# Kernel tuning notes

Measured on AMD Instinct MI355X. Metric: run time of the kernel, lower is better.

Reference implementation:

```python
import jax, jax.numpy as jnp
import numpy as np
import math

NUM_IN_C = 128      # rep_2d num_c (c_z)
ATT_C = 64          # attention_num_c
NUM_HEADS = 4
B, T, I, J = 1, 4, 256, 256


def setup_inputs() -> dict:
    key = jax.random.key(0)
    ks = jax.random.split(key, 7)
    s = 1.0 / math.sqrt(NUM_IN_C)
    return {
        "z2d": jax.random.normal(ks[0], (B, I, J, NUM_IN_C), dtype=jnp.float32),
        "t2d": jax.random.normal(ks[1], (B, T, I, J, NUM_IN_C), dtype=jnp.float32),
        # nn.Linear weights are [out_features, in_features]; apply as x @ W.T
        "Wq": jax.random.normal(ks[2], (ATT_C * NUM_HEADS, NUM_IN_C), dtype=jnp.float32) * s,
        "Wk": jax.random.normal(ks[3], (ATT_C * NUM_HEADS, NUM_IN_C), dtype=jnp.float32) * s,
        "Wv": jax.random.normal(ks[4], (ATT_C * NUM_HEADS, NUM_IN_C), dtype=jnp.float32) * s,
        "Wo": jax.random.normal(ks[5], (NUM_IN_C, ATT_C * NUM_HEADS), dtype=jnp.float32) * s,
        "bo": jax.random.normal(ks[6], (NUM_IN_C,), dtype=jnp.float32) * 0.02,
    }


def reference(z2d, t2d, Wq, Wk, Wv, Wo, bo):
    # Projections; reshape last dim to (attention_num_c, num_heads) per torch .view
    q = (z2d @ Wq.T).reshape(*z2d.shape[:-1], ATT_C, NUM_HEADS)        # b i j c h
    k = (t2d @ Wk.T).reshape(*t2d.shape[:-1], ATT_C, NUM_HEADS)        # b t i j c h
    v = (t2d @ Wv.T).reshape(*t2d.shape[:-1], ATT_C, NUM_HEADS)        # b t i j c h
    # NOTE: original scales by sqrt(num_in_c), not sqrt(attention_num_c)
    scores = jnp.einsum('bijch,btijch->btijh', q, k) / math.sqrt(NUM_IN_C)
    w = jax.nn.softmax(scores, axis=1)                                  # softmax over template axis t
    out = jnp.einsum('btijh,btijch->bijch', w, v)                       # b i j c h
    out = out.reshape(*out.shape[:-2], ATT_C * NUM_HEADS)               # flatten (c,h)
    return out @ Wo.T + bo
```

## Files before the change

### kernel.cpp

```cpp
#include <hip/hip_runtime.h>


#define PIX 65536
#define MT 32

typedef __attribute__((ext_vector_type(8))) short s8v;
typedef __attribute__((ext_vector_type(4))) float f4v;
typedef __attribute__((ext_vector_type(4))) unsigned short us4v;
typedef __attribute__((ext_vector_type(4))) float fl4;

__device__ __forceinline__ unsigned short f2bf(float x) {
    unsigned int u = __float_as_uint(x);
    u = (u + 0x7FFFu + ((u >> 16) & 1u)) >> 16;
    return (unsigned short)u;
}
__device__ __forceinline__ float bf2fs(short v) {
    return __uint_as_float(((unsigned int)(unsigned short)v) << 16);
}

__global__ __launch_bounds__(256) void build_weights(
        const float* __restrict__ Wq, const float* __restrict__ Wk,
        const float* __restrict__ Wv, const float* __restrict__ Wo,
        unsigned short* __restrict__ mcat, unsigned short* __restrict__ pcat) {
    int b = blockIdx.x;
    if (b < 256) {
        int idx = b * 256 + threadIdx.x;
        int n = idx >> 7, k1 = idx & 127;
        int h = n >> 7, k2 = n & 127;
        float s = 0.f;
        #pragma unroll 8
        for (int c = 0; c < 64; c++) {
            int r = c * 4 + h;
            s += Wq[r * 128 + k1] * Wk[r * 128 + k2];
        }
        mcat[idx] = f2bf(s * 0.088388347648318447f);
    } else {
        int idx = (b - 256) * 256 + threadIdx.x;
        int m = idx >> 9, kk = idx & 511;
        int h = kk >> 7, k = kk & 127;
        float s = 0.f;
        #pragma unroll 8
        for (int c = 0; c < 64; c++) {
            int r = c * 4 + h;
            s += Wo[m * 256 + r] * Wv[r * 128 + k];
        }
        pcat[idx] = f2bf(s);
    }
}

#define AT_OFS 0
#define U_OFS  17408
#define BUF_USH (17408 + 16768)

__global__ __launch_bounds__(256, 2) void fused_attn(
    const float* __restrict__ z2d, const float* __restrict__ t2d,
    const unsigned short* __restrict__ mcat, const unsigned short* __restrict__ pcat,
    const float* __restrict__ bo, float* __restrict__ out) {

    __shared__ unsigned short buf[BUF_USH];
    __shared__ float Sc[4][32][4];

    const int tid = threadIdx.x;
    const int pbase = blockIdx.x * MT;
    const int wv = tid >> 6, lane = tid & 63, quad = lane >> 4, l15 = lane & 15;
    const int mt = wv & 1;
    const int nsel = wv >> 1;

    s8v za[4];
    {
        const float* zp = z2d + (size_t)(pbase + mt * 16 + l15) * 128 + quad * 8;
        #pragma unroll
        for (int ks = 0; ks < 4; ks++) {
            const fl4 d0 = *(const fl4*)(zp + ks * 32);
            const fl4 d1 = *(const fl4*)(zp + ks * 32 + 4);
            s8v a;
            a[0] = (short)f2bf(d0[0]); a[1] = (short)f2bf(d0[1]);
            a[2] = (short)f2bf(d0[2]); a[3] = (short)f2bf(d0[3]);
            a[4] = (short)f2bf(d1[0]); a[5] = (short)f2bf(d1[1]);
            a[6] = (short)f2bf(d1[2]); a[7] = (short)f2bf(d1[3]);
            za[ks] = a;
        }
    }

    for (int v = tid; v < 4096; v += 256) {
        int t = v >> 10, rem = v & 1023, p = rem >> 5, k4 = (rem & 31) << 2;
        const fl4 d = *(const fl4*)(t2d + ((size_t)t * PIX + pbase + p) * 128 + k4);
        us4v w;
        w[0] = f2bf(d[0]); w[1] = f2bf(d[1]); w[2] = f2bf(d[2]); w[3] = f2bf(d[3]);
        *(us4v*)&buf[AT_OFS + (t * 32 + p) * 136 + k4] = w;
    }
    __syncthreads();

    for (int nblk = 0; nblk < 8; nblk++) {
        s8v b0[4], b1[4];
        #pragma unroll
        for (int ks = 0; ks < 4; ks++) {
            b0[ks] = *(const s8v*)(mcat + (size_t)(nblk * 64 + nsel * 32 + l15) * 128
                                        + ks * 32 + quad * 8);
            b1[ks] = *(const s8v*)(mcat + (size_t)(nblk * 64 + nsel * 32 + 16 + l15) * 128
                                        + ks * 32 + quad * 8);
        }
        f4v acc0 = {0.f, 0.f, 0.f, 0.f}, acc1 = {0.f, 0.f, 0.f, 0.f};
        #pragma unroll
        for (int ks = 0; ks < 4; ks++) {
            acc0 = __builtin_amdgcn_mfma_f32_16x16x32_bf16(za[ks], b0[ks], acc0, 0, 0, 0);
            acc1 = __builtin_amdgcn_mfma_f32_16x16x32_bf16(za[ks], b1[ks], acc1, 0, 0, 0);
        }
        const int prow = mt * 16 + quad * 4;
        const int cb = nblk * 64 + nsel * 32 + l15;
        #pragma unroll
        for (int r = 0; r < 4; r++) {
            buf[U_OFS + (prow + r) * 524 + cb]      = f2bf(acc0[r]);
            buf[U_OFS + (prow + r) * 524 + cb + 16] = f2bf(acc1[r]);
        }
    }
    __syncthreads();

    {
        const int t = wv;
        #pragma unroll
        for (int pt = 0; pt < 2; pt++) {
            s8v bt[4];
            #pragma unroll
            for (int ks = 0; ks < 4; ks++)
                bt[ks] = *(const s8v*)&buf[AT_OFS + (t * 32 + pt * 16 + l15) * 136
                                            + ks * 32 + quad * 8];
            #pragma unroll
            for (int h = 0; h < 4; h++) {
                f4v c = {0.f, 0.f, 0.f, 0.f};
                #pragma unroll
                for (int ks = 0; ks < 4; ks++) {
                    const s8v a = *(const s8v*)&buf[U_OFS + (pt * 16 + l15) * 524
                                                     + h * 128 + ks * 32 + quad * 8];
                    c = __builtin_amdgcn_mfma_f32_16x16x32_bf16(a, bt[ks], c, 0, 0, 0);
                }
                const int rsel = l15 & 3;
                float dv = rsel == 0 ? c[0] : rsel == 1 ? c[1] : rsel == 2 ? c[2] : c[3];
                if ((l15 >> 2) == quad) Sc[t][pt * 16 + l15][h] = dv;
            }
        }
    }
    __syncthreads();

    if (tid < 128) {
        const int p = tid >> 2, h = tid & 3;
        float x0 = Sc[0][p][h], x1 = Sc[1][p][h], x2 = Sc[2][p][h], x3 = Sc[3][p][h];
        float mx = fmaxf(fmaxf(x0, x1), fmaxf(x2, x3));
        float e0 = __expf(x0 - mx), e1 = __expf(x1 - mx);
        float e2 = __expf(x2 - mx), e3 = __expf(x3 - mx);
        float inv = 1.f / (e0 + e1 + e2 + e3);
        Sc[0][p][h] = e0 * inv; Sc[1][p][h] = e1 * inv;
        Sc[2][p][h] = e2 * inv; Sc[3][p][h] = e3 * inv;
    }
    __syncthreads();

    {
        const int p = tid >> 3, seg = tid & 7;
        float w[4][4];
        #pragma unroll
        for (int t = 0; t < 4; t++) {
            const fl4 ww = *(const fl4*)&Sc[t][p][0];
            w[t][0] = ww[0]; w[t][1] = ww[1]; w[t][2] = ww[2]; w[t][3] = ww[3];
        }
        #pragma unroll
        for (int half = 0; half < 2; half++) {
            const int k = seg * 16 + half * 8;
            s8v a[4];
            #pragma unroll
            for (int t = 0; t < 4; t++)
                a[t] = *(const s8v*)&buf[AT_OFS + (t * 32 + p) * 136 + k];
            s8v o[4];
            #pragma unroll
            for (int j = 0; j < 8; j++) {
                const float a0 = bf2fs(a[0][j]), a1 = bf2fs(a[1][j]);
                const float a2 = bf2fs(a[2][j]), a3 = bf2fs(a[3][j]);
                #pragma unroll
                for (int h = 0; h < 4; h++) {
                    o[h][j] = (short)f2bf(w[0][h] * a0 + w[1][h] * a1
                                        + w[2][h] * a2 + w[3][h] * a3);
                }
            }
            #pragma unroll
            for (int h = 0; h < 4; h++)
                *(s8v*)&buf[AT_OFS + (h * 32 + p) * 136 + k] = o[h];
        }
    }
    __syncthreads();

    f4v accd[4];
    #pragma unroll
    for (int i = 0; i < 4; i++) accd[i] = (f4v){0.f, 0.f, 0.f, 0.f};
    #pragma unroll
    for (int h = 0; h < 4; h++) {
        s8v af[4];
        #pragma unroll
        for (int ks = 0; ks < 4; ks++)
            af[ks] = *(const s8v*)&buf[AT_OFS + (h * 32 + mt * 16 + l15) * 136
                                        + ks * 32 + quad * 8];
        #pragma unroll
        for (int nt = 0; nt < 4; nt++) {
            #pragma unroll
            for (int ks = 0; ks < 4; ks++) {
                const s8v b = *(const s8v*)(pcat + (size_t)(nsel * 64 + nt * 16 + l15) * 512
                                                 + h * 128 + ks * 32 + quad * 8);
                accd[nt] = __builtin_amdgcn_mfma_f32_16x16x32_bf16(af[ks], b, accd[nt], 0, 0, 0);
            }
        }
    }

    const int prow2 = mt * 16 + quad * 4;
    #pragma unroll
    for (int nt = 0; nt < 4; nt++) {
        const int m = nsel * 64 + nt * 16 + l15;
        const float bb = bo[m];
        #pragma unroll
        for (int r = 0; r < 4; r++) {
            out[(size_t)(pbase + prow2 + r) * 128 + m] = accd[nt][r] + bb;
        }
    }
}

extern "C" void kernel_launch(void* const* d_in, const int* in_sizes, int n_in,
                              void* d_out, int out_size, void* d_ws, size_t ws_size,
                              hipStream_t stream) {
    const float* z2d = (const float*)d_in[0];
    const float* t2d = (const float*)d_in[1];
    const float* Wq  = (const float*)d_in[2];
    const float* Wk  = (const float*)d_in[3];
    const float* Wv  = (const float*)d_in[4];
    const float* Wo  = (const float*)d_in[5];
    const float* bo  = (const float*)d_in[6];

    unsigned short* mcat = (unsigned short*)d_ws;
    unsigned short* pcat = mcat + 512 * 128;

    build_weights<<<512, 256, 0, stream>>>(Wq, Wk, Wv, Wo, mcat, pcat);
    fused_attn<<<PIX / MT, 256, 0, stream>>>(z2d, t2d, mcat, pcat, bo, (float*)d_out);
}
```

Measured before the change: 343.5 us.

## Halve pixel tile per block and raise occupancy to four blocks per CU

Shrinks the per-block pixel tile from 32 to 16, halving shared memory use, and raises the launch-bounds target from 2 to 4 blocks per CU. The warp-to-work mapping is reorganised so each wave covers all 16 pixels with its own column slice in the projection and output GEMMs. The t2d load loop is fully unrolled. The aim is more resident waves to hide global-load latency, at the cost of reloading weight fragments (mcat/pcat) twice as often per pixel and giving each wave less MFMA work.

```diff
diff --git a/kernel.cpp b/kernel.cpp
--- a/kernel.cpp
+++ b/kernel.cpp
@@ -2,7 +2,7 @@
 
 
 #define PIX 65536
-#define MT 32
+#define MT 16
 
 typedef __attribute__((ext_vector_type(8))) short s8v;
 typedef __attribute__((ext_vector_type(4))) float f4v;
@@ -49,26 +49,24 @@
 }
 
 #define AT_OFS 0
-#define U_OFS  17408
-#define BUF_USH (17408 + 16768)
-
-__global__ __launch_bounds__(256, 2) void fused_attn(
+#define U_OFS  8704
+#define BUF_USH (8704 + 8384)
+
+__global__ __launch_bounds__(256, 4) void fused_attn(
     const float* __restrict__ z2d, const float* __restrict__ t2d,
     const unsigned short* __restrict__ mcat, const unsigned short* __restrict__ pcat,
     const float* __restrict__ bo, float* __restrict__ out) {
 
     __shared__ unsigned short buf[BUF_USH];
-    __shared__ float Sc[4][32][4];
+    __shared__ float Sc[4][16][4];
 
     const int tid = threadIdx.x;
     const int pbase = blockIdx.x * MT;
     const int wv = tid >> 6, lane = tid & 63, quad = lane >> 4, l15 = lane & 15;
-    const int mt = wv & 1;
-    const int nsel = wv >> 1;
 
     s8v za[4];
     {
-        const float* zp = z2d + (size_t)(pbase + mt * 16 + l15) * 128 + quad * 8;
+        const float* zp = z2d + (size_t)(pbase + l15) * 128 + quad * 8;
         #pragma unroll
         for (int ks = 0; ks < 4; ks++) {
             const fl4 d0 = *(const fl4*)(zp + ks * 32);
@@ -82,67 +80,57 @@
         }
     }
 
-    for (int v = tid; v < 4096; v += 256) {
-        int t = v >> 10, rem = v & 1023, p = rem >> 5, k4 = (rem & 31) << 2;
+    #pragma unroll
+    for (int i = 0; i < 8; i++) {
+        int v = i * 256 + tid;
+        int t = v >> 9, rem = v & 511, p = rem >> 5, k4 = (rem & 31) << 2;
         const fl4 d = *(const fl4*)(t2d + ((size_t)t * PIX + pbase + p) * 128 + k4);
         us4v w;
         w[0] = f2bf(d[0]); w[1] = f2bf(d[1]); w[2] = f2bf(d[2]); w[3] = f2bf(d[3]);
-        *(us4v*)&buf[AT_OFS + (t * 32 + p) * 136 + k4] = w;
-    }
-    __syncthreads();
-
-    for (int nblk = 0; nblk < 8; nblk++) {
-        s8v b0[4], b1[4];
-        #pragma unroll
-        for (int ks = 0; ks < 4; ks++) {
-            b0[ks] = *(const s8v*)(mcat + (size_t)(nblk * 64 + nsel * 32 + l15) * 128
-                                        + ks * 32 + quad * 8);
-            b1[ks] = *(const s8v*)(mcat + (size_t)(nblk * 64 + nsel * 32 + 16 + l15) * 128
-                                        + ks * 32 + quad * 8);
-        }
-        f4v acc0 = {0.f, 0.f, 0.f, 0.f}, acc1 = {0.f, 0.f, 0.f, 0.f};
-        #pragma unroll
-        for (int ks = 0; ks < 4; ks++) {
-            acc0 = __builtin_amdgcn_mfma_f32_16x16x32_bf16(za[ks], b0[ks], acc0, 0, 0, 0);
-            acc1 = __builtin_amdgcn_mfma_f32_16x16x32_bf16(za[ks], b1[ks], acc1, 0, 0, 0);
-        }
-        const int prow = mt * 16 + quad * 4;
-        const int cb = nblk * 64 + nsel * 32 + l15;
-        #pragma unroll
-        for (int r = 0; r < 4; r++) {
-            buf[U_OFS + (prow + r) * 524 + cb]      = f2bf(acc0[r]);
-            buf[U_OFS + (prow + r) * 524 + cb + 16] = f2bf(acc1[r]);
-        }
+        *(us4v*)&buf[AT_OFS + (t * 16 + p) * 136 + k4] = w;
+    }
+    __syncthreads();
+
+    #pragma unroll
+    for (int cb = 0; cb < 8; cb++) {
+        const int col = wv * 128 + cb * 16 + l15;
+        s8v b[4];
+        #pragma unroll
+        for (int ks = 0; ks < 4; ks++)
+            b[ks] = *(const s8v*)(mcat + (size_t)col * 128 + ks * 32 + quad * 8);
+        f4v acc = {0.f, 0.f, 0.f, 0.f};
+        #pragma unroll
+        for (int ks = 0; ks < 4; ks++)
+            acc = __builtin_amdgcn_mfma_f32_16x16x32_bf16(za[ks], b[ks], acc, 0, 0, 0);
+        #pragma unroll
+        for (int r = 0; r < 4; r++)
+            buf[U_OFS + (quad * 4 + r) * 524 + col] = f2bf(acc[r]);
     }
     __syncthreads();
 
     {
         const int t = wv;
-        #pragma unroll
-        for (int pt = 0; pt < 2; pt++) {
-            s8v bt[4];
+        s8v bt[4];
+        #pragma unroll
+        for (int ks = 0; ks < 4; ks++)
+            bt[ks] = *(const s8v*)&buf[AT_OFS + (t * 16 + l15) * 136 + ks * 32 + quad * 8];
+        #pragma unroll
+        for (int h = 0; h < 4; h++) {
+            f4v c = {0.f, 0.f, 0.f, 0.f};
             #pragma unroll
-            for (int ks = 0; ks < 4; ks++)
-                bt[ks] = *(const s8v*)&buf[AT_OFS + (t * 32 + pt * 16 + l15) * 136
-                                            + ks * 32 + quad * 8];
-            #pragma unroll
-            for (int h = 0; h < 4; h++) {
-                f4v c = {0.f, 0.f, 0.f, 0.f};
-                #pragma unroll
-                for (int ks = 0; ks < 4; ks++) {
-                    const s8v a = *(const s8v*)&buf[U_OFS + (pt * 16 + l15) * 524
-                                                     + h * 128 + ks * 32 + quad * 8];
-                    c = __builtin_amdgcn_mfma_f32_16x16x32_bf16(a, bt[ks], c, 0, 0, 0);
-                }
-                const int rsel = l15 & 3;
-                float dv = rsel == 0 ? c[0] : rsel == 1 ? c[1] : rsel == 2 ? c[2] : c[3];
-                if ((l15 >> 2) == quad) Sc[t][pt * 16 + l15][h] = dv;
+            for (int ks = 0; ks < 4; ks++) {
+                const s8v a = *(const s8v*)&buf[U_OFS + l15 * 524
+                                                 + h * 128 + ks * 32 + quad * 8];
+                c = __builtin_amdgcn_mfma_f32_16x16x32_bf16(a, bt[ks], c, 0, 0, 0);
             }
-        }
-    }
-    __syncthreads();
-
-    if (tid < 128) {
+            const int rsel = l15 & 3;
+            float dv = rsel == 0 ? c[0] : rsel == 1 ? c[1] : rsel == 2 ? c[2] : c[3];
+            if ((l15 >> 2) == quad) Sc[t][l15][h] = dv;
+        }
+    }
+    __syncthreads();
+
+    if (tid < 64) {
         const int p = tid >> 2, h = tid & 3;
         float x0 = Sc[0][p][h], x1 = Sc[1][p][h], x2 = Sc[2][p][h], x3 = Sc[3][p][h];
         float mx = fmaxf(fmaxf(x0, x1), fmaxf(x2, x3));
@@ -155,67 +143,61 @@
     __syncthreads();
 
     {
-        const int p = tid >> 3, seg = tid & 7;
+        const int p = tid >> 4, seg = tid & 15, k = seg * 8;
         float w[4][4];
         #pragma unroll
         for (int t = 0; t < 4; t++) {
             const fl4 ww = *(const fl4*)&Sc[t][p][0];
             w[t][0] = ww[0]; w[t][1] = ww[1]; w[t][2] = ww[2]; w[t][3] = ww[3];
         }
-        #pragma unroll
-        for (int half = 0; half < 2; half++) {
-            const int k = seg * 16 + half * 8;
-            s8v a[4];
+        s8v a[4];
+        #pragma unroll
+        for (int t = 0; t < 4; t++)
+            a[t] = *(const s8v*)&buf[AT_OFS + (t * 16 + p) * 136 + k];
+        s8v o[4];
+        #pragma unroll
+        for (int j = 0; j < 8; j++) {
+            const float a0 = bf2fs(a[0][j]), a1 = bf2fs(a[1][j]);
+            const float a2 = bf2fs(a[2][j]), a3 = bf2fs(a[3][j]);
             #pragma unroll
-            for (int t = 0; t < 4; t++)
-                a[t] = *(const s8v*)&buf[AT_OFS + (t * 32 + p) * 136 + k];
-            s8v o[4];
-            #pragma unroll
-            for (int j = 0; j < 8; j++) {
-                const float a0 = bf2fs(a[0][j]), a1 = bf2fs(a[1][j]);
-                const float a2 = bf2fs(a[2][j]), a3 = bf2fs(a[3][j]);
-                #pragma unroll
-                for (int h = 0; h < 4; h++) {
-                    o[h][j] = (short)f2bf(w[0][h] * a0 + w[1][h] * a1
-                                        + w[2][h] * a2 + w[3][h] * a3);
-                }
+            for (int h = 0; h < 4; h++) {
+                o[h][j] = (short)f2bf(w[0][h] * a0 + w[1][h] * a1
+                                    + w[2][h] * a2 + w[3][h] * a3);
             }
-            #pragma unroll
-            for (int h = 0; h < 4; h++)
-                *(s8v*)&buf[AT_OFS + (h * 32 + p) * 136 + k] = o[h];
-        }
-    }
-    __syncthreads();
-
-    f4v accd[4];
-    #pragma unroll
-    for (int i = 0; i < 4; i++) accd[i] = (f4v){0.f, 0.f, 0.f, 0.f};
+        }
+        #pragma unroll
+        for (int h = 0; h < 4; h++)
+            *(s8v*)&buf[AT_OFS + (h * 16 + p) * 136 + k] = o[h];
+    }
+    __syncthreads();
+
+    f4v accd[2];
+    accd[0] = (f4v){0.f, 0.f, 0.f, 0.f};
+    accd[1] = (f4v){0.f, 0.f, 0.f, 0.f};
     #pragma unroll
     for (int h = 0; h < 4; h++) {
         s8v af[4];
         #pragma unroll
         for (int ks = 0; ks < 4; ks++)
-            af[ks] = *(const s8v*)&buf[AT_OFS + (h * 32 + mt * 16 + l15) * 136
-                                        + ks * 32 + quad * 8];
-        #pragma unroll
-        for (int nt = 0; nt < 4; nt++) {
+            af[ks] = *(const s8v*)&buf[AT_OFS + (h * 16 + l15) * 136 + ks * 32 + quad * 8];
+        #pragma unroll
+        for (int nt = 0; nt < 2; nt++) {
             #pragma unroll
             for (int ks = 0; ks < 4; ks++) {
-                const s8v b = *(const s8v*)(pcat + (size_t)(nsel * 64 + nt * 16 + l15) * 512
+                const s8v b = *(const s8v*)(pcat + (size_t)(wv * 32 + nt * 16 + l15) * 512
                                                  + h * 128 + ks * 32 + quad * 8);
                 accd[nt] = __builtin_amdgcn_mfma_f32_16x16x32_bf16(af[ks], b, accd[nt], 0, 0, 0);
             }
         }
     }
 
-    const int prow2 = mt * 16 + quad * 4;
-    #pragma unroll
-    for (int nt = 0; nt < 4; nt++) {
-        const int m = nsel * 64 + nt * 16 + l15;
+    #pragma unroll
+    for (int nt = 0; nt < 2; nt++) {
+        const int m = wv * 32 + nt * 16 + l15;
         const float bb = bo[m];
         #pragma unroll
         for (int r = 0; r < 4; r++) {
-            out[(size_t)(pbase + prow2 + r) * 128 + m] = accd[nt][r] + bb;
+            out[(size_t)(pbase + quad * 4 + r) * 128 + m] = accd[nt][r] + bb;
         }
     }
 }
```

Result: faster. 325.2 us (-5.3%).
